# Kernel tuning notes

Hardware: AMD Instinct MI355X
Metric: run time of the kernel (lower is better)

The kernel has to match this reference:

```python
import jax, jax.numpy as jnp
import numpy as np

B, T, E, H = 4, 1024, 512, 8
DH = E // H  # head dim = 64


def setup_inputs() -> dict:
    key = jax.random.key(0)
    ks = jax.random.split(key, 6)
    s = 1.0 / np.sqrt(E)
    return {
        "q": jax.random.normal(ks[0], (B, T, E), dtype=jnp.float32),
        "kv": jax.random.normal(ks[1], (B, T, E), dtype=jnp.float32),
        "Wq": jax.random.normal(ks[2], (E, E), dtype=jnp.float32) * s,
        "Wk": jax.random.normal(ks[3], (E, E), dtype=jnp.float32) * s,
        "Wv": jax.random.normal(ks[4], (E, E), dtype=jnp.float32) * s,
        "Wo": jax.random.normal(ks[5], (E, E), dtype=jnp.float32) * s,
        "head_num": H,
    }


def _split_heads_dh(x, h):
    # einops 'b t (d h)' with h=head_num: head index is FASTEST in channel dim
    b, t, e = x.shape
    d = e // h
    return x.reshape(b, t, d, h).transpose(0, 3, 1, 2)  # (b, h, t, d)


def reference(q, kv, Wq, Wk, Wv, Wo, head_num):
    e = q.shape[-1]
    dk = (e // head_num) ** 0.5  # NOTE: multiplied, per original code

    qp = q @ Wq   # weights stored as (in, out); Linear(bias=False)
    kp = kv @ Wk
    vp = kv @ Wv

    query = _split_heads_dh(qp, head_num)  # (b, h, t, d)
    key = _split_heads_dh(kp, head_num)
    value = _split_heads_dh(vp, head_num)

    qf = jnp.fft.fftn(query, axes=(-2, -1))  # complex, over (t, d)
    kf = jnp.fft.fftn(key, axes=(-2, -1))

    # complex einsum, key NOT conjugated (faithful to torch source)
    energy = jnp.einsum("bhid,bhjd->bhij", qf, kf) * dk
    energy = jnp.fft.ifftn(energy, axes=(-2, -1)).real  # (b, h, t, t)

    attention = jax.nn.softmax(energy, axis=-1)
    out = jnp.einsum("bhij,bhjd->bhid", attention, value)  # (b, h, t, d)

    # einops 'b h t d -> b t (h d)': head index SLOWEST in output channel dim
    b, h, t, d = out.shape
    out = out.transpose(0, 2, 1, 3).reshape(b, t, h * d)
    return out @ Wo
```

## Files before the change

### kernel.cpp

```cpp
#include <hip/hip_runtime.h>
#include <math.h>

#define BB 4
#define TT 1024
#define EE 512
#define HH 8
#define DD 64
#define BT (BB * TT)

typedef _Float16 f16;
typedef __attribute__((ext_vector_type(8))) _Float16 f16x8;
typedef __attribute__((ext_vector_type(4))) float f32x4;

__global__ __launch_bounds__(256) void prep_w_k(const float* __restrict__ Wq,
    const float* __restrict__ Wk, const float* __restrict__ Wv,
    const float* __restrict__ Wo,
    f16* __restrict__ wqh, f16* __restrict__ wql,
    f16* __restrict__ wkh, f16* __restrict__ wkl,
    f16* __restrict__ wvh, f16* __restrict__ woh) {
    int idx = blockIdx.x * 256 + threadIdx.x;
    int k = idx & (EE - 1);
    int n = idx >> 9;
    int which = blockIdx.y;
    if (which == 0) {
        float v = Wq[k * EE + n] * 512.0f;
        f16 hi = (f16)v;
        wqh[n * EE + k] = hi;
        wql[n * EE + k] = (f16)(v - (float)hi);
    } else if (which == 1) {
        int d = n >> 3, h = n & 7;
        int sn = (((DD - d) & (DD - 1)) << 3) | h;
        float v = Wk[k * EE + sn];
        f16 hi = (f16)v;
        wkh[n * EE + k] = hi;
        wkl[n * EE + k] = (f16)(v - (float)hi);
    } else if (which == 2) {
        wvh[n * EE + k] = (f16)Wv[k * EE + n];
    } else {
        woh[n * EE + k] = (f16)Wo[k * EE + n];
    }
}

template<int ASPLIT, int WSPLIT, int SMODE>
__global__ __launch_bounds__(256) void mm_k(const void* __restrict__ Aptr,
                                            const f16* __restrict__ WThi,
                                            const f16* __restrict__ WTlo,
                                            void* __restrict__ Out0,
                                            f16* __restrict__ Out1) {
    __shared__ __align__(16) f16 Ah_s[2][64][40];
    __shared__ __align__(16) f16 Al_s[ASPLIT == 2 ? 2 : 1][ASPLIT == 2 ? 64 : 1][40];
    __shared__ __align__(16) f16 Wh_s[2][64][40];
    __shared__ __align__(16) f16 Wl_s[WSPLIT ? 2 : 1][WSPLIT ? 64 : 1][40];
    __shared__ __align__(16) f16 Ep[SMODE ? 64 : 1][72];

    const int t = threadIdx.x;
    const int w = t >> 6, l = t & 63;
    const int wm = w >> 1, wn = w & 1;
    const int fr = l & 15, fc = l >> 4;
    const int m0b = blockIdx.x * 64;
    const int n0b = blockIdx.y * 64;
    const int sr = t >> 2, sch = t & 3;

    f32x4 acc[2][2];
#pragma unroll
    for (int i = 0; i < 2; ++i)
#pragma unroll
        for (int j = 0; j < 2; ++j) acc[i][j] = f32x4{0.f, 0.f, 0.f, 0.f};

    float4 a4x[2];
    f16x8 af, wh8, wl8;

    auto loadAB = [&](int k0) {
        if (ASPLIT >= 1) {
            const float* A = (const float*)Aptr;
            const float* src = A + (size_t)(m0b + sr) * EE + k0 + sch * 8;
            a4x[0] = ((const float4*)src)[0];
            a4x[1] = ((const float4*)src)[1];
        } else {
            const f16* A = (const f16*)Aptr;
            af = *(const f16x8*)&A[(size_t)(m0b + sr) * EE + k0 + sch * 8];
        }
        wh8 = *(const f16x8*)&WThi[(size_t)(n0b + sr) * EE + k0 + sch * 8];
        if (WSPLIT)
            wl8 = *(const f16x8*)&WTlo[(size_t)(n0b + sr) * EE + k0 + sch * 8];
    };
    auto stage = [&](int bf) {
        if (ASPLIT >= 1) {
            float xs[8] = {a4x[0].x, a4x[0].y, a4x[0].z, a4x[0].w,
                           a4x[1].x, a4x[1].y, a4x[1].z, a4x[1].w};
            f16x8 hi, lo;
#pragma unroll
            for (int e = 0; e < 8; ++e) {
                f16 hh = (f16)xs[e];
                hi[e] = hh;
                if (ASPLIT == 2) lo[e] = (f16)(xs[e] - (float)hh);
            }
            *(f16x8*)&Ah_s[bf][sr][sch * 8] = hi;
            if (ASPLIT == 2) *(f16x8*)&Al_s[bf][sr][sch * 8] = lo;
        } else {
            *(f16x8*)&Ah_s[bf][sr][sch * 8] = af;
        }
        *(f16x8*)&Wh_s[bf][sr][sch * 8] = wh8;
        if (WSPLIT) *(f16x8*)&Wl_s[bf][sr][sch * 8] = wl8;
    };

    loadAB(0);
    stage(0);
    __syncthreads();
    int cur = 0;
    for (int ks = 0; ks < 16; ++ks) {
        if (ks < 15) loadAB((ks + 1) * 32);
        f16x8 Ahf[2], Alf[2], Bhf[2], Blf[2];
#pragma unroll
        for (int mi = 0; mi < 2; ++mi) {
            Ahf[mi] = *(const f16x8*)&Ah_s[cur][wm * 32 + mi * 16 + fr][fc * 8];
            if (ASPLIT == 2)
                Alf[mi] = *(const f16x8*)&Al_s[cur][wm * 32 + mi * 16 + fr][fc * 8];
        }
#pragma unroll
        for (int nj = 0; nj < 2; ++nj) {
            Bhf[nj] = *(const f16x8*)&Wh_s[cur][wn * 32 + nj * 16 + fr][fc * 8];
            if (WSPLIT)
                Blf[nj] = *(const f16x8*)&Wl_s[cur][wn * 32 + nj * 16 + fr][fc * 8];
        }
        __builtin_amdgcn_s_setprio(1);
#pragma unroll
        for (int mi = 0; mi < 2; ++mi)
#pragma unroll
            for (int nj = 0; nj < 2; ++nj) {
                acc[mi][nj] = __builtin_amdgcn_mfma_f32_16x16x32_f16(
                    Ahf[mi], Bhf[nj], acc[mi][nj], 0, 0, 0);
                if (WSPLIT)
                    acc[mi][nj] = __builtin_amdgcn_mfma_f32_16x16x32_f16(
                        Ahf[mi], Blf[nj], acc[mi][nj], 0, 0, 0);
                if (ASPLIT == 2)
                    acc[mi][nj] = __builtin_amdgcn_mfma_f32_16x16x32_f16(
                        Alf[mi], Bhf[nj], acc[mi][nj], 0, 0, 0);
            }
        __builtin_amdgcn_s_setprio(0);
        if (ks < 15) stage(cur ^ 1);
        __syncthreads();
        cur ^= 1;
    }

    if (SMODE == 0) {
        float* out = (float*)Out0;
#pragma unroll
        for (int mi = 0; mi < 2; ++mi)
#pragma unroll
            for (int nj = 0; nj < 2; ++nj)
#pragma unroll
                for (int r = 0; r < 4; ++r)
                    out[(size_t)(m0b + wm * 32 + mi * 16 + fc * 4 + r) * EE +
                        n0b + wn * 32 + nj * 16 + fr] = acc[mi][nj][r];
        return;
    }

    __syncthreads();
#pragma unroll
    for (int mi = 0; mi < 2; ++mi)
#pragma unroll
        for (int nj = 0; nj < 2; ++nj)
#pragma unroll
            for (int r = 0; r < 4; ++r)
                Ep[wn * 32 + nj * 16 + fr][wm * 32 + mi * 16 + fc * 4 + r] =
                    (f16)acc[mi][nj][r];
    __syncthreads();
    if (SMODE == 1) {
        f16* dhi = (f16*)Out0;
#pragma unroll
        for (int i = 0; i < 2; ++i) {
            int task = t * 2 + i;
            int mr = task >> 3, h = task & 7;
            f16x8 v;
#pragma unroll
            for (int d = 0; d < 8; ++d) v[d] = Ep[8 * d + h][mr];
            *(f16x8*)&dhi[((size_t)h * BT + m0b + mr) * DD + (n0b >> 3)] = v;
        }
        __syncthreads();
#pragma unroll
        for (int mi = 0; mi < 2; ++mi)
#pragma unroll
            for (int nj = 0; nj < 2; ++nj)
#pragma unroll
                for (int r = 0; r < 4; ++r) {
                    float x = acc[mi][nj][r];
                    f16 hh = (f16)x;
                    Ep[wn * 32 + nj * 16 + fr][wm * 32 + mi * 16 + fc * 4 + r] =
                        (f16)(x - (float)hh);
                }
        __syncthreads();
#pragma unroll
        for (int i = 0; i < 2; ++i) {
            int task = t * 2 + i;
            int mr = task >> 3, h = task & 7;
            f16x8 v;
#pragma unroll
            for (int d = 0; d < 8; ++d) v[d] = Ep[8 * d + h][mr];
            *(f16x8*)&Out1[((size_t)h * BT + m0b + mr) * DD + (n0b >> 3)] = v;
        }
    } else {
        f16* dst = (f16*)Out0;
#pragma unroll
        for (int i = 0; i < 2; ++i) {
            int task = t * 2 + i;
            int mg = task & 7, nn = task >> 3;
            int h = nn & 7, dl = nn >> 3;
            f16x8 v = *(const f16x8*)&Ep[nn][mg * 8];
            *(f16x8*)&dst[((size_t)(h * DD + (n0b >> 3) + dl)) * BT +
                          m0b + mg * 8] = v;
        }
    }
}

__global__ __launch_bounds__(256) void attn_mfma_k(const f16* __restrict__ qhiP,
    const f16* __restrict__ qloP, const f16* __restrict__ khiP,
    const f16* __restrict__ kloP, const f16* __restrict__ vTP,
    f16* __restrict__ ctx) {
    __shared__ __align__(16) f16 Khi[2][64][64];
    __shared__ __align__(16) f16 Klo[2][64][64];
    __shared__ __align__(16) f16 VT[2][64][72];
    __shared__ __align__(16) f16 Pl[4][16][88];

    const int t  = threadIdx.x;
    const int w  = t >> 6;
    const int l  = t & 63;
    const int lg = l >> 4;
    const int lq = l & 15;
    const int q0 = blockIdx.x * 64 + w * 16;
    const int h  = blockIdx.y;
    const int b  = blockIdx.z;
    const size_t plane = ((size_t)h * BT + (size_t)b * TT) * DD;

    f16x8 Qhi[2], Qlo[2];
#pragma unroll
    for (int kf = 0; kf < 2; ++kf) {
        size_t qo = plane + (size_t)(q0 + lq) * DD + kf * 32 + lg * 8;
        Qhi[kf] = *(const f16x8*)&qhiP[qo];
        Qlo[kf] = *(const f16x8*)&qloP[qo];
    }

    f32x4 Oacc[4];
#pragma unroll
    for (int i = 0; i < 4; ++i) Oacc[i] = f32x4{0.f, 0.f, 0.f, 0.f};
    float m = -1e30f, lsum = 0.f;

    const int sr = t >> 2, sch = t & 3;
    f16x8 kh[2], kl[2], vv[2];

    auto loadKV = [&](int kt0) {
        size_t off = plane + (size_t)(kt0 + sr) * DD + sch * 16;
        kh[0] = *(const f16x8*)&khiP[off];
        kh[1] = *(const f16x8*)&khiP[off + 8];
        kl[0] = *(const f16x8*)&kloP[off];
        kl[1] = *(const f16x8*)&kloP[off + 8];
        size_t voff = ((size_t)h * DD + sr) * BT + (size_t)b * TT + kt0 + sch * 16;
        vv[0] = *(const f16x8*)&vTP[voff];
        vv[1] = *(const f16x8*)&vTP[voff + 8];
    };
    auto stageKV = [&](int bf) {
#pragma unroll
        for (int i = 0; i < 2; ++i) {
            int chunk = sch * 2 + i;
            int dsw = chunk ^ (sr & 7);
            *(f16x8*)&Khi[bf][sr][dsw * 8] = kh[i];
            *(f16x8*)&Klo[bf][sr][dsw * 8] = kl[i];
            *(f16x8*)&VT[bf][sr][chunk * 8] = vv[i];
        }
    };

    loadKV(0);
    stageKV(0);
    __syncthreads();
    int cur = 0;

    for (int kt0 = 0; kt0 < TT; kt0 += 64) {
        if (kt0 + 64 < TT) loadKV(kt0 + 64);

        f32x4 Sc[4];
        __builtin_amdgcn_s_setprio(1);
#pragma unroll
        for (int kt = 0; kt < 4; ++kt) {
            f32x4 c = f32x4{0.f, 0.f, 0.f, 0.f};
            int keyr = kt * 16 + lq;
#pragma unroll
            for (int kf = 0; kf < 2; ++kf) {
                int dblk = kf * 4 + lg;
                int sw = dblk ^ (keyr & 7);
                f16x8 ahi = *(const f16x8*)&Khi[cur][keyr][sw * 8];
                f16x8 alo = *(const f16x8*)&Klo[cur][keyr][sw * 8];
                c = __builtin_amdgcn_mfma_f32_16x16x32_f16(ahi, Qhi[kf], c, 0, 0, 0);
                c = __builtin_amdgcn_mfma_f32_16x16x32_f16(ahi, Qlo[kf], c, 0, 0, 0);
                c = __builtin_amdgcn_mfma_f32_16x16x32_f16(alo, Qhi[kf], c, 0, 0, 0);
            }
            Sc[kt] = c;
        }
        __builtin_amdgcn_s_setprio(0);

        float s[16];
#pragma unroll
        for (int kt = 0; kt < 4; ++kt)
#pragma unroll
            for (int r = 0; r < 4; ++r) s[kt * 4 + r] = Sc[kt][r];
        float tm = s[0];
#pragma unroll
        for (int i = 1; i < 16; ++i) tm = fmaxf(tm, s[i]);
        tm = fmaxf(tm, __shfl_xor(tm, 16));
        tm = fmaxf(tm, __shfl_xor(tm, 32));

        bool skip = __all(tm <= m + 8.0f);
        float Mn = m, corr = 1.0f;
        if (!skip) {
            Mn = fmaxf(m, tm);
            corr = __expf(m - Mn);
        }
        float ps = 0.f;
        f16 ph[16];
#pragma unroll
        for (int i = 0; i < 16; ++i) {
            float p = __expf(s[i] - Mn);
            ps += p;
            ph[i] = (f16)p;
        }
        ps += __shfl_xor(ps, 16);
        ps += __shfl_xor(ps, 32);
        if (skip) {
            lsum += ps;
        } else {
            lsum = lsum * corr + ps;
            m = Mn;
        }

#pragma unroll
        for (int kt = 0; kt < 4; ++kt)
#pragma unroll
            for (int rp = 0; rp < 4; rp += 2) {
                union { f16 h; unsigned short u; } u0, u1;
                u0.h = ph[kt * 4 + rp]; u1.h = ph[kt * 4 + rp + 1];
                unsigned int pk = ((unsigned int)u1.u << 16) | u0.u;
                *(unsigned int*)&Pl[w][lq][kt * 16 + lg * 4 + rp] = pk;
            }

        if (!skip) {
            float cq[4];
#pragma unroll
            for (int r = 0; r < 4; ++r) cq[r] = __shfl(corr, lg * 4 + r);
#pragma unroll
            for (int dvt = 0; dvt < 4; ++dvt)
#pragma unroll
                for (int r = 0; r < 4; ++r) Oacc[dvt][r] *= cq[r];
        }

        __builtin_amdgcn_s_setprio(1);
#pragma unroll
        for (int kf = 0; kf < 2; ++kf) {
            f16x8 pa = *(const f16x8*)&Pl[w][lq][kf * 32 + lg * 8];
#pragma unroll
            for (int dvt = 0; dvt < 4; ++dvt) {
                f16x8 bv = *(const f16x8*)&VT[cur][dvt * 16 + lq][kf * 32 + lg * 8];
                Oacc[dvt] = __builtin_amdgcn_mfma_f32_16x16x32_f16(pa, bv, Oacc[dvt], 0, 0, 0);
            }
        }
        __builtin_amdgcn_s_setprio(0);

        if (kt0 + 64 < TT) stageKV(cur ^ 1);
        __syncthreads();
        cur ^= 1;
    }

    float linv = 1.0f / lsum;
    float lq4[4];
#pragma unroll
    for (int r = 0; r < 4; ++r) lq4[r] = __shfl(linv, lg * 4 + r);
#pragma unroll
    for (int r = 0; r < 4; ++r) {
        f16* crow = ctx + (size_t)(b * TT + q0 + lg * 4 + r) * EE + h * DD;
#pragma unroll
        for (int dvt = 0; dvt < 4; ++dvt)
            crow[dvt * 16 + lq] = (f16)(Oacc[dvt][r] * lq4[r]);
    }
}

extern "C" void kernel_launch(void* const* d_in, const int* in_sizes, int n_in,
                              void* d_out, int out_size, void* d_ws, size_t ws_size,
                              hipStream_t stream) {
    const float* q  = (const float*)d_in[0];
    const float* kv = (const float*)d_in[1];
    const float* Wq = (const float*)d_in[2];
    const float* Wk = (const float*)d_in[3];
    const float* Wv = (const float*)d_in[4];
    const float* Wo = (const float*)d_in[5];
    float* out = (float*)d_out;

    f16* ws = (f16*)d_ws;
    const size_t PL  = (size_t)HH * BT * DD;
    const size_t WPL = (size_t)EE * EE;
    f16* qhi = ws + 0 * PL;
    f16* qlo = ws + 1 * PL;
    f16* khi = ws + 2 * PL;
    f16* klo = ws + 3 * PL;
    f16* vT  = ws + 4 * PL;
    f16* ctx = ws + 5 * PL;
    f16* wqh = ws + 6 * PL;
    f16* wql = wqh + 1 * WPL;
    f16* wkh = wqh + 2 * WPL;
    f16* wkl = wqh + 3 * WPL;
    f16* wvh = wqh + 4 * WPL;
    f16* woh = wqh + 5 * WPL;

    prep_w_k<<<dim3((EE * EE) / 256, 4), dim3(256), 0, stream>>>(
        Wq, Wk, Wv, Wo, wqh, wql, wkh, wkl, wvh, woh);

    dim3 ggrid(BT / 64, EE / 64);
    mm_k<2, 1, 1><<<ggrid, dim3(256), 0, stream>>>(q,  wqh, wql, qhi, qlo);
    mm_k<2, 1, 1><<<ggrid, dim3(256), 0, stream>>>(kv, wkh, wkl, khi, klo);
    mm_k<1, 0, 2><<<ggrid, dim3(256), 0, stream>>>(kv, wvh, nullptr, vT, nullptr);

    attn_mfma_k<<<dim3(TT / 64, HH, BB), dim3(256), 0, stream>>>(
        qhi, qlo, khi, klo, vT, ctx);

    mm_k<0, 0, 0><<<ggrid, dim3(256), 0, stream>>>(ctx, woh, nullptr, out, nullptr);
}
```

Before: 92.39 us.

## Fuse Q/K/V projections into one launch sharing kv tiles; widen output GEMM k-step

```diff
diff --git a/kernel.cpp b/kernel.cpp
--- a/kernel.cpp
+++ b/kernel.cpp
@@ -41,17 +41,179 @@
     }
 }
 
-template<int ASPLIT, int WSPLIT, int SMODE>
-__global__ __launch_bounds__(256) void mm_k(const void* __restrict__ Aptr,
-                                            const f16* __restrict__ WThi,
-                                            const f16* __restrict__ WTlo,
-                                            void* __restrict__ Out0,
-                                            f16* __restrict__ Out1) {
+__global__ __launch_bounds__(256) void proj_k(
+    const float* __restrict__ qA, const float* __restrict__ kvA,
+    const f16* __restrict__ wqh, const f16* __restrict__ wql,
+    const f16* __restrict__ wkh, const f16* __restrict__ wkl,
+    const f16* __restrict__ wvh,
+    f16* __restrict__ qhi, f16* __restrict__ qlo,
+    f16* __restrict__ khi, f16* __restrict__ klo, f16* __restrict__ vT) {
     __shared__ __align__(16) f16 Ah_s[2][64][40];
-    __shared__ __align__(16) f16 Al_s[ASPLIT == 2 ? 2 : 1][ASPLIT == 2 ? 64 : 1][40];
+    __shared__ __align__(16) f16 Al_s[2][64][40];
     __shared__ __align__(16) f16 Wh_s[2][64][40];
-    __shared__ __align__(16) f16 Wl_s[WSPLIT ? 2 : 1][WSPLIT ? 64 : 1][40];
-    __shared__ __align__(16) f16 Ep[SMODE ? 64 : 1][72];
+    __shared__ __align__(16) f16 Wl_s[2][64][40];
+    __shared__ __align__(16) f16 Wv_s[2][64][40];
+    __shared__ __align__(16) f16 Ep[64][72];
+
+    const int t = threadIdx.x;
+    const int w = t >> 6, l = t & 63;
+    const int wm = w >> 1, wn = w & 1;
+    const int fr = l & 15, fc = l >> 4;
+    const int m0b = blockIdx.x * 64;
+    const int n0b = blockIdx.y * 64;
+    const int z   = blockIdx.z;
+    const int sr = t >> 2, sch = t & 3;
+
+    const float* A  = z ? kvA : qA;
+    const f16*   WH = z ? wkh : wqh;
+    const f16*   WL = z ? wkl : wql;
+
+    f32x4 accK[2][2], accV[2][2];
+#pragma unroll
+    for (int i = 0; i < 2; ++i)
+#pragma unroll
+        for (int j = 0; j < 2; ++j) {
+            accK[i][j] = f32x4{0.f, 0.f, 0.f, 0.f};
+            accV[i][j] = f32x4{0.f, 0.f, 0.f, 0.f};
+        }
+
+    float4 a4x[2];
+    f16x8 wh8, wl8, wv8;
+
+    auto loadAB = [&](int k0) {
+        const float* src = A + (size_t)(m0b + sr) * EE + k0 + sch * 8;
+        a4x[0] = ((const float4*)src)[0];
+        a4x[1] = ((const float4*)src)[1];
+        wh8 = *(const f16x8*)&WH[(size_t)(n0b + sr) * EE + k0 + sch * 8];
+        wl8 = *(const f16x8*)&WL[(size_t)(n0b + sr) * EE + k0 + sch * 8];
+        if (z) wv8 = *(const f16x8*)&wvh[(size_t)(n0b + sr) * EE + k0 + sch * 8];
+    };
+    auto stage = [&](int bf) {
+        float xs[8] = {a4x[0].x, a4x[0].y, a4x[0].z, a4x[0].w,
+                       a4x[1].x, a4x[1].y, a4x[1].z, a4x[1].w};
+        f16x8 hi, lo;
+#pragma unroll
+        for (int e = 0; e < 8; ++e) {
+            f16 hh = (f16)xs[e];
+            hi[e] = hh;
+            lo[e] = (f16)(xs[e] - (float)hh);
+        }
+        *(f16x8*)&Ah_s[bf][sr][sch * 8] = hi;
+        *(f16x8*)&Al_s[bf][sr][sch * 8] = lo;
+        *(f16x8*)&Wh_s[bf][sr][sch * 8] = wh8;
+        *(f16x8*)&Wl_s[bf][sr][sch * 8] = wl8;
+        if (z) *(f16x8*)&Wv_s[bf][sr][sch * 8] = wv8;
+    };
+
+    loadAB(0);
+    stage(0);
+    __syncthreads();
+    int cur = 0;
+    for (int ks = 0; ks < 16; ++ks) {
+        if (ks < 15) loadAB((ks + 1) * 32);
+        f16x8 Ahf[2], Alf[2], Bh[2], Bl[2], Bv[2];
+#pragma unroll
+        for (int mi = 0; mi < 2; ++mi) {
+            Ahf[mi] = *(const f16x8*)&Ah_s[cur][wm * 32 + mi * 16 + fr][fc * 8];
+            Alf[mi] = *(const f16x8*)&Al_s[cur][wm * 32 + mi * 16 + fr][fc * 8];
+        }
+#pragma unroll
+        for (int nj = 0; nj < 2; ++nj) {
+            Bh[nj] = *(const f16x8*)&Wh_s[cur][wn * 32 + nj * 16 + fr][fc * 8];
+            Bl[nj] = *(const f16x8*)&Wl_s[cur][wn * 32 + nj * 16 + fr][fc * 8];
+            if (z) Bv[nj] = *(const f16x8*)&Wv_s[cur][wn * 32 + nj * 16 + fr][fc * 8];
+        }
+        __builtin_amdgcn_s_setprio(1);
+#pragma unroll
+        for (int mi = 0; mi < 2; ++mi)
+#pragma unroll
+            for (int nj = 0; nj < 2; ++nj) {
+                accK[mi][nj] = __builtin_amdgcn_mfma_f32_16x16x32_f16(
+                    Ahf[mi], Bh[nj], accK[mi][nj], 0, 0, 0);
+                accK[mi][nj] = __builtin_amdgcn_mfma_f32_16x16x32_f16(
+                    Ahf[mi], Bl[nj], accK[mi][nj], 0, 0, 0);
+                accK[mi][nj] = __builtin_amdgcn_mfma_f32_16x16x32_f16(
+                    Alf[mi], Bh[nj], accK[mi][nj], 0, 0, 0);
+                if (z)
+                    accV[mi][nj] = __builtin_amdgcn_mfma_f32_16x16x32_f16(
+                        Ahf[mi], Bv[nj], accV[mi][nj], 0, 0, 0);
+            }
+        __builtin_amdgcn_s_setprio(0);
+        if (ks < 15) stage(cur ^ 1);
+        __syncthreads();
+        cur ^= 1;
+    }
+
+    f16* dsthi = z ? khi : qhi;
+    f16* dstlo = z ? klo : qlo;
+#pragma unroll
+    for (int mi = 0; mi < 2; ++mi)
+#pragma unroll
+        for (int nj = 0; nj < 2; ++nj)
+#pragma unroll
+            for (int r = 0; r < 4; ++r)
+                Ep[wn * 32 + nj * 16 + fr][wm * 32 + mi * 16 + fc * 4 + r] =
+                    (f16)accK[mi][nj][r];
+    __syncthreads();
+#pragma unroll
+    for (int i = 0; i < 2; ++i) {
+        int task = t * 2 + i;
+        int mr = task >> 3, h = task & 7;
+        f16x8 v;
+#pragma unroll
+        for (int d = 0; d < 8; ++d) v[d] = Ep[8 * d + h][mr];
+        *(f16x8*)&dsthi[((size_t)h * BT + m0b + mr) * DD + (n0b >> 3)] = v;
+    }
+    __syncthreads();
+#pragma unroll
+    for (int mi = 0; mi < 2; ++mi)
+#pragma unroll
+        for (int nj = 0; nj < 2; ++nj)
+#pragma unroll
+            for (int r = 0; r < 4; ++r) {
+                float x = accK[mi][nj][r];
+                f16 hh = (f16)x;
+                Ep[wn * 32 + nj * 16 + fr][wm * 32 + mi * 16 + fc * 4 + r] =
+                    (f16)(x - (float)hh);
+            }
+    __syncthreads();
+#pragma unroll
+    for (int i = 0; i < 2; ++i) {
+        int task = t * 2 + i;
+        int mr = task >> 3, h = task & 7;
+        f16x8 v;
+#pragma unroll
+        for (int d = 0; d < 8; ++d) v[d] = Ep[8 * d + h][mr];
+        *(f16x8*)&dstlo[((size_t)h * BT + m0b + mr) * DD + (n0b >> 3)] = v;
+    }
+    if (z) {
+        __syncthreads();
+#pragma unroll
+        for (int mi = 0; mi < 2; ++mi)
+#pragma unroll
+            for (int nj = 0; nj < 2; ++nj)
+#pragma unroll
+                for (int r = 0; r < 4; ++r)
+                    Ep[wn * 32 + nj * 16 + fr][wm * 32 + mi * 16 + fc * 4 + r] =
+                        (f16)accV[mi][nj][r];
+        __syncthreads();
+#pragma unroll
+        for (int i = 0; i < 2; ++i) {
+            int task = t * 2 + i;
+            int mg = task & 7, nn = task >> 3;
+            int h = nn & 7, dl = nn >> 3;
+            f16x8 v = *(const f16x8*)&Ep[nn][mg * 8];
+            *(f16x8*)&vT[((size_t)(h * DD + (n0b >> 3) + dl)) * BT +
+                         m0b + mg * 8] = v;
+        }
+    }
+}
+
+__global__ __launch_bounds__(256) void outmm_k(const f16* __restrict__ Af,
+                                               const f16* __restrict__ WThi,
+                                               float* __restrict__ out) {
+    __shared__ __align__(16) f16 Ah_s[2][64][72];
+    __shared__ __align__(16) f16 Wh_s[2][64][72];
 
     const int t = threadIdx.x;
     const int w = t >> 6, l = t & 63;
@@ -67,150 +229,65 @@
 #pragma unroll
         for (int j = 0; j < 2; ++j) acc[i][j] = f32x4{0.f, 0.f, 0.f, 0.f};
 
-    float4 a4x[2];
-    f16x8 af, wh8, wl8;
-
+    f16x8 af[2], wf[2];
     auto loadAB = [&](int k0) {
-        if (ASPLIT >= 1) {
-            const float* A = (const float*)Aptr;
-            const float* src = A + (size_t)(m0b + sr) * EE + k0 + sch * 8;
-            a4x[0] = ((const float4*)src)[0];
-            a4x[1] = ((const float4*)src)[1];
-        } else {
-            const f16* A = (const f16*)Aptr;
-            af = *(const f16x8*)&A[(size_t)(m0b + sr) * EE + k0 + sch * 8];
-        }
-        wh8 = *(const f16x8*)&WThi[(size_t)(n0b + sr) * EE + k0 + sch * 8];
-        if (WSPLIT)
-            wl8 = *(const f16x8*)&WTlo[(size_t)(n0b + sr) * EE + k0 + sch * 8];
+#pragma unroll
+        for (int i = 0; i < 2; ++i) {
+            af[i] = *(const f16x8*)&Af[(size_t)(m0b + sr) * EE + k0 + sch * 16 + i * 8];
+            wf[i] = *(const f16x8*)&WThi[(size_t)(n0b + sr) * EE + k0 + sch * 16 + i * 8];
+        }
     };
     auto stage = [&](int bf) {
-        if (ASPLIT >= 1) {
-            float xs[8] = {a4x[0].x, a4x[0].y, a4x[0].z, a4x[0].w,
-                           a4x[1].x, a4x[1].y, a4x[1].z, a4x[1].w};
-            f16x8 hi, lo;
-#pragma unroll
-            for (int e = 0; e < 8; ++e) {
-                f16 hh = (f16)xs[e];
-                hi[e] = hh;
-                if (ASPLIT == 2) lo[e] = (f16)(xs[e] - (float)hh);
-            }
-            *(f16x8*)&Ah_s[bf][sr][sch * 8] = hi;
-            if (ASPLIT == 2) *(f16x8*)&Al_s[bf][sr][sch * 8] = lo;
-        } else {
-            *(f16x8*)&Ah_s[bf][sr][sch * 8] = af;
-        }
-        *(f16x8*)&Wh_s[bf][sr][sch * 8] = wh8;
-        if (WSPLIT) *(f16x8*)&Wl_s[bf][sr][sch * 8] = wl8;
+#pragma unroll
+        for (int i = 0; i < 2; ++i) {
+            *(f16x8*)&Ah_s[bf][sr][sch * 16 + i * 8] = af[i];
+            *(f16x8*)&Wh_s[bf][sr][sch * 16 + i * 8] = wf[i];
+        }
     };
 
     loadAB(0);
     stage(0);
     __syncthreads();
     int cur = 0;
-    for (int ks = 0; ks < 16; ++ks) {
-        if (ks < 15) loadAB((ks + 1) * 32);
-        f16x8 Ahf[2], Alf[2], Bhf[2], Blf[2];
-#pragma unroll
-        for (int mi = 0; mi < 2; ++mi) {
-            Ahf[mi] = *(const f16x8*)&Ah_s[cur][wm * 32 + mi * 16 + fr][fc * 8];
-            if (ASPLIT == 2)
-                Alf[mi] = *(const f16x8*)&Al_s[cur][wm * 32 + mi * 16 + fr][fc * 8];
-        }
-#pragma unroll
-        for (int nj = 0; nj < 2; ++nj) {
-            Bhf[nj] = *(const f16x8*)&Wh_s[cur][wn * 32 + nj * 16 + fr][fc * 8];
-            if (WSPLIT)
-                Blf[nj] = *(const f16x8*)&Wl_s[cur][wn * 32 + nj * 16 + fr][fc * 8];
-        }
+    for (int ks = 0; ks < 8; ++ks) {
+        if (ks < 7) loadAB((ks + 1) * 64);
+        f16x8 Ahf[2][2], Bhf[2][2];
+#pragma unroll
+        for (int mi = 0; mi < 2; ++mi)
+#pragma unroll
+            for (int kb = 0; kb < 2; ++kb)
+                Ahf[mi][kb] =
+                    *(const f16x8*)&Ah_s[cur][wm * 32 + mi * 16 + fr][kb * 32 + fc * 8];
+#pragma unroll
+        for (int nj = 0; nj < 2; ++nj)
+#pragma unroll
+            for (int kb = 0; kb < 2; ++kb)
+                Bhf[nj][kb] =
+                    *(const f16x8*)&Wh_s[cur][wn * 32 + nj * 16 + fr][kb * 32 + fc * 8];
         __builtin_amdgcn_s_setprio(1);
 #pragma unroll
         for (int mi = 0; mi < 2; ++mi)
 #pragma unroll
-            for (int nj = 0; nj < 2; ++nj) {
-                acc[mi][nj] = __builtin_amdgcn_mfma_f32_16x16x32_f16(
-                    Ahf[mi], Bhf[nj], acc[mi][nj], 0, 0, 0);
-                if (WSPLIT)
+            for (int nj = 0; nj < 2; ++nj)
+#pragma unroll
+                for (int kb = 0; kb < 2; ++kb)
                     acc[mi][nj] = __builtin_amdgcn_mfma_f32_16x16x32_f16(
-                        Ahf[mi], Blf[nj], acc[mi][nj], 0, 0, 0);
-                if (ASPLIT == 2)
-                    acc[mi][nj] = __builtin_amdgcn_mfma_f32_16x16x32_f16(
-                        Alf[mi], Bhf[nj], acc[mi][nj], 0, 0, 0);
-            }
+                        Ahf[mi][kb], Bhf[nj][kb], acc[mi][nj], 0, 0, 0);
         __builtin_amdgcn_s_setprio(0);
-        if (ks < 15) stage(cur ^ 1);
+        if (ks < 7) stage(cur ^ 1);
         __syncthreads();
         cur ^= 1;
     }
 
-    if (SMODE == 0) {
-        float* out = (float*)Out0;
-#pragma unroll
-        for (int mi = 0; mi < 2; ++mi)
-#pragma unroll
-            for (int nj = 0; nj < 2; ++nj)
-#pragma unroll
-                for (int r = 0; r < 4; ++r)
-                    out[(size_t)(m0b + wm * 32 + mi * 16 + fc * 4 + r) * EE +
-                        n0b + wn * 32 + nj * 16 + fr] = acc[mi][nj][r];
-        return;
-    }
-
-    __syncthreads();
+    float* o = out;
 #pragma unroll
     for (int mi = 0; mi < 2; ++mi)
 #pragma unroll
         for (int nj = 0; nj < 2; ++nj)
 #pragma unroll
             for (int r = 0; r < 4; ++r)
-                Ep[wn * 32 + nj * 16 + fr][wm * 32 + mi * 16 + fc * 4 + r] =
-                    (f16)acc[mi][nj][r];
-    __syncthreads();
-    if (SMODE == 1) {
-        f16* dhi = (f16*)Out0;
-#pragma unroll
-        for (int i = 0; i < 2; ++i) {
-            int task = t * 2 + i;
-            int mr = task >> 3, h = task & 7;
-            f16x8 v;
-#pragma unroll
-            for (int d = 0; d < 8; ++d) v[d] = Ep[8 * d + h][mr];
-            *(f16x8*)&dhi[((size_t)h * BT + m0b + mr) * DD + (n0b >> 3)] = v;
-        }
-        __syncthreads();
-#pragma unroll
-        for (int mi = 0; mi < 2; ++mi)
-#pragma unroll
-            for (int nj = 0; nj < 2; ++nj)
-#pragma unroll
-                for (int r = 0; r < 4; ++r) {
-                    float x = acc[mi][nj][r];
-                    f16 hh = (f16)x;
-                    Ep[wn * 32 + nj * 16 + fr][wm * 32 + mi * 16 + fc * 4 + r] =
-                        (f16)(x - (float)hh);
-                }
-        __syncthreads();
-#pragma unroll
-        for (int i = 0; i < 2; ++i) {
-            int task = t * 2 + i;
-            int mr = task >> 3, h = task & 7;
-            f16x8 v;
-#pragma unroll
-            for (int d = 0; d < 8; ++d) v[d] = Ep[8 * d + h][mr];
-            *(f16x8*)&Out1[((size_t)h * BT + m0b + mr) * DD + (n0b >> 3)] = v;
-        }
-    } else {
-        f16* dst = (f16*)Out0;
-#pragma unroll
-        for (int i = 0; i < 2; ++i) {
-            int task = t * 2 + i;
-            int mg = task & 7, nn = task >> 3;
-            int h = nn & 7, dl = nn >> 3;
-            f16x8 v = *(const f16x8*)&Ep[nn][mg * 8];
-            *(f16x8*)&dst[((size_t)(h * DD + (n0b >> 3) + dl)) * BT +
-                          m0b + mg * 8] = v;
-        }
-    }
+                o[(size_t)(m0b + wm * 32 + mi * 16 + fc * 4 + r) * EE +
+                  n0b + wn * 32 + nj * 16 + fr] = acc[mi][nj][r];
 }
 
 __global__ __launch_bounds__(256) void attn_mfma_k(const f16* __restrict__ qhiP,
@@ -411,13 +488,11 @@
     prep_w_k<<<dim3((EE * EE) / 256, 4), dim3(256), 0, stream>>>(
         Wq, Wk, Wv, Wo, wqh, wql, wkh, wkl, wvh, woh);
 
-    dim3 ggrid(BT / 64, EE / 64);
-    mm_k<2, 1, 1><<<ggrid, dim3(256), 0, stream>>>(q,  wqh, wql, qhi, qlo);
-    mm_k<2, 1, 1><<<ggrid, dim3(256), 0, stream>>>(kv, wkh, wkl, khi, klo);
-    mm_k<1, 0, 2><<<ggrid, dim3(256), 0, stream>>>(kv, wvh, nullptr, vT, nullptr);
+    proj_k<<<dim3(BT / 64, EE / 64, 2), dim3(256), 0, stream>>>(
+        q, kv, wqh, wql, wkh, wkl, wvh, qhi, qlo, khi, klo, vT);
 
     attn_mfma_k<<<dim3(TT / 64, HH, BB), dim3(256), 0, stream>>>(
         qhi, qlo, khi, klo, vT, ctx);
 
-    mm_k<0, 0, 0><<<ggrid, dim3(256), 0, stream>>>(ctx, woh, nullptr, out, nullptr);
+    outmm_k<<<dim3(BT / 64, EE / 64), dim3(256), 0, stream>>>(ctx, woh, out);
 }
```

Result: faster. 83.94 us (-9.1%).
